# Kernel tuning notes

Hardware: AMD Instinct MI355X
Metric: run time of the kernel (lower is better)

## Reference

```python
import jax, jax.numpy as jnp
import numpy as np
import math

DIM = 1024
HEADS = 16
HEAD_DIM = DIM // HEADS
B, N = 1, 4096


def setup_inputs() -> dict:
    key = jax.random.key(0)
    k1, k2, k3, k4 = jax.random.split(key, 4)
    content = jax.random.normal(k1, (B, N, DIM), dtype=jnp.float32)
    # Original initializes projections as identity; perturb slightly so the
    # projections are non-trivial while staying well-conditioned.
    Wq = jnp.eye(DIM, dtype=jnp.float32) + 0.02 * jax.random.normal(k2, (DIM, DIM), dtype=jnp.float32)
    Wk = jnp.eye(DIM, dtype=jnp.float32) + 0.02 * jax.random.normal(k3, (DIM, DIM), dtype=jnp.float32)
    Wv = jnp.eye(DIM, dtype=jnp.float32) + 0.02 * jax.random.normal(k4, (DIM, DIM), dtype=jnp.float32)
    return {"content": content, "Wq": Wq, "Wk": Wk, "Wv": Wv}


def reference(content, Wq, Wk, Wv):
    b, n, d = content.shape
    # QKV projections: [B,N,D] @ [D,D]
    Q = (content @ Wq).reshape(b, n, HEADS, HEAD_DIM)
    K = (content @ Wk).reshape(b, n, HEADS, HEAD_DIM)
    V = (content @ Wv).reshape(b, n, HEADS, HEAD_DIM)
    # torch.split along the last dim == reshape into [.., HEADS, HEAD_DIM]
    scores = jnp.einsum('bqhd,bkhd->bhqk', Q, K) / math.sqrt(HEAD_DIM)
    alpha = jax.nn.softmax(scores, axis=-1)
    # Faithful to the original: masking zeroes the upper triangle AFTER the
    # softmax (no renormalization). With B=1 this applies to the whole batch,
    # exactly as the original loop (which only touches batch index 0).
    causal = jnp.tril(jnp.ones((n, n), dtype=bool))
    alpha = jnp.where(causal, alpha, jnp.zeros((), dtype=alpha.dtype))
    Y = jnp.einsum('bhqk,bkhd->bqhd', alpha, V).reshape(b, n, d)
    return Y
```

## Files before the change

### kernel.cpp

```cpp
#include <hip/hip_runtime.h>
#include <stdint.h>

#define DIMC 1024
#define NSEQ 4096
#define NH 16

typedef __attribute__((ext_vector_type(8))) short bf16x8;
typedef __attribute__((ext_vector_type(4))) float f32x4;

__device__ __forceinline__ unsigned short f2bf(float x) {
    union { float f; unsigned int u; } v; v.f = x;
    unsigned int u = v.u;
    return (unsigned short)((u + 0x7fffu + ((u >> 16) & 1u)) >> 16);
}

__global__ __launch_bounds__(256) void k_conv(const float* __restrict__ in,
                                              unsigned short* __restrict__ out) {
    int i = (blockIdx.x * 256 + threadIdx.x) * 8;
    float4 a = *reinterpret_cast<const float4*>(in + i);
    float4 b = *reinterpret_cast<const float4*>(in + i + 4);
    union { unsigned short us[8]; uint4 v; } r;
    r.us[0] = f2bf(a.x); r.us[1] = f2bf(a.y); r.us[2] = f2bf(a.z); r.us[3] = f2bf(a.w);
    r.us[4] = f2bf(b.x); r.us[5] = f2bf(b.y); r.us[6] = f2bf(b.z); r.us[7] = f2bf(b.w);
    *reinterpret_cast<uint4*>(out + i) = r.v;
}

__global__ __launch_bounds__(1024) void k_wt(const float* __restrict__ Wq,
                                             const float* __restrict__ Wk,
                                             const float* __restrict__ Wv,
                                             unsigned short* __restrict__ wt) {
    __shared__ float tile[32][33];
    int z = blockIdx.z;
    const float* W = (z == 0) ? Wq : ((z == 1) ? Wk : Wv);
    int n0 = blockIdx.x * 32, k0 = blockIdx.y * 32;
    tile[threadIdx.y][threadIdx.x] = W[(k0 + threadIdx.y) * DIMC + n0 + threadIdx.x];
    __syncthreads();
    wt[(size_t)z * DIMC * DIMC + (n0 + threadIdx.y) * DIMC + k0 + threadIdx.x] =
        f2bf(tile[threadIdx.x][threadIdx.y]);
}

__global__ __launch_bounds__(256) void k_gemm(const unsigned short* __restrict__ A,
                                              const unsigned short* __restrict__ Wt,
                                              unsigned short* __restrict__ Qb,
                                              unsigned short* __restrict__ Kb,
                                              unsigned short* __restrict__ Vt) {
    __shared__ unsigned short As[128][40];
    __shared__ unsigned short Bs[128][40];
    const int z = blockIdx.z;
    const unsigned short* Wz = Wt + (size_t)z * DIMC * DIMC;
    const int n0 = blockIdx.x * 128, m0 = blockIdx.y * 128;
    const int t = threadIdx.x;
    const int w = t >> 6, l = t & 63;
    const int wr = w >> 1, wc = w & 1;
    const int lq = l & 15, lg = l >> 4;
    const int srow = t >> 1, sch = (t & 1) * 16;

    f32x4 acc[4][4];
    #pragma unroll
    for (int i = 0; i < 4; ++i)
        #pragma unroll
        for (int j = 0; j < 4; ++j)
            acc[i][j] = f32x4{0.f, 0.f, 0.f, 0.f};

    for (int k0 = 0; k0 < DIMC; k0 += 32) {
        uint4 va0 = *reinterpret_cast<const uint4*>(A  + (m0 + srow) * DIMC + k0 + sch);
        uint4 va1 = *reinterpret_cast<const uint4*>(A  + (m0 + srow) * DIMC + k0 + sch + 8);
        uint4 vb0 = *reinterpret_cast<const uint4*>(Wz + (n0 + srow) * DIMC + k0 + sch);
        uint4 vb1 = *reinterpret_cast<const uint4*>(Wz + (n0 + srow) * DIMC + k0 + sch + 8);
        __syncthreads();
        *reinterpret_cast<uint4*>(&As[srow][sch])     = va0;
        *reinterpret_cast<uint4*>(&As[srow][sch + 8]) = va1;
        *reinterpret_cast<uint4*>(&Bs[srow][sch])     = vb0;
        *reinterpret_cast<uint4*>(&Bs[srow][sch + 8]) = vb1;
        __syncthreads();
        bf16x8 af[4], bfr[4];
        #pragma unroll
        for (int mf = 0; mf < 4; ++mf)
            af[mf] = *reinterpret_cast<const bf16x8*>(&As[wr * 64 + mf * 16 + lq][lg * 8]);
        #pragma unroll
        for (int nf = 0; nf < 4; ++nf)
            bfr[nf] = *reinterpret_cast<const bf16x8*>(&Bs[wc * 64 + nf * 16 + lq][lg * 8]);
        #pragma unroll
        for (int mf = 0; mf < 4; ++mf)
            #pragma unroll
            for (int nf = 0; nf < 4; ++nf)
                acc[mf][nf] = __builtin_amdgcn_mfma_f32_16x16x32_bf16(af[mf], bfr[nf], acc[mf][nf], 0, 0, 0);
    }

    if (z < 2) {
        unsigned short* out = (z == 0) ? Qb : Kb;
        #pragma unroll
        for (int mf = 0; mf < 4; ++mf)
            #pragma unroll
            for (int nf = 0; nf < 4; ++nf)
                #pragma unroll
                for (int j = 0; j < 4; ++j) {
                    int row = m0 + wr * 64 + mf * 16 + lg * 4 + j;
                    int col = n0 + wc * 64 + nf * 16 + lq;
                    out[row * DIMC + col] = f2bf(acc[mf][nf][j]);
                }
    } else {
        #pragma unroll
        for (int mf = 0; mf < 4; ++mf)
            #pragma unroll
            for (int nf = 0; nf < 4; ++nf) {
                int row  = n0 + wc * 64 + nf * 16 + lq;
                int colb = m0 + wr * 64 + mf * 16 + lg * 4;
                uint2 pk;
                pk.x = (unsigned)f2bf(acc[mf][nf][0]) | ((unsigned)f2bf(acc[mf][nf][1]) << 16);
                pk.y = (unsigned)f2bf(acc[mf][nf][2]) | ((unsigned)f2bf(acc[mf][nf][3]) << 16);
                *reinterpret_cast<uint2*>(Vt + (size_t)row * NSEQ + colb) = pk;
            }
    }
}

__global__ __launch_bounds__(256) void k_attn(const unsigned short* __restrict__ Qb,
                                              const unsigned short* __restrict__ Kb,
                                              const unsigned short* __restrict__ Vt,
                                              float* __restrict__ Y) {
    __shared__ unsigned short Ks[64][72];
    __shared__ unsigned short Vs[64][72];
    __shared__ unsigned short Ps[4][16][72];
    const int qb = blockIdx.x, h = blockIdx.y;
    const int t = threadIdx.x;
    const int w = t >> 6, l = t & 63;
    const int lq = l & 15, lg = l >> 4;

    bf16x8 qf0, qf1;
    {
        const unsigned short* qp = Qb + (qb * 64 + w * 16 + lq) * DIMC + h * 64 + lg * 8;
        qf0 = *reinterpret_cast<const bf16x8*>(qp);
        qf1 = *reinterpret_cast<const bf16x8*>(qp + 32);
    }
    float m_st = -__builtin_inff(), l_st = 0.f;
    float m_pv = -__builtin_inff();
    f32x4 O[4];
    #pragma unroll
    for (int df = 0; df < 4; ++df) O[df] = f32x4{0.f, 0.f, 0.f, 0.f};

    const int r0 = t >> 3, c0 = (t & 7) * 8;

    for (int kt = 0; kt < 64; ++kt) {
        const bool pv = (kt <= qb);
        uint4 kv0 = *reinterpret_cast<const uint4*>(Kb + (kt * 64 + r0) * DIMC + h * 64 + c0);
        uint4 kv1 = *reinterpret_cast<const uint4*>(Kb + (kt * 64 + 32 + r0) * DIMC + h * 64 + c0);
        uint4 vv0, vv1;
        if (pv) {
            vv0 = *reinterpret_cast<const uint4*>(Vt + (size_t)(h * 64 + r0) * NSEQ + kt * 64 + c0);
            vv1 = *reinterpret_cast<const uint4*>(Vt + (size_t)(h * 64 + 32 + r0) * NSEQ + kt * 64 + c0);
        }
        __syncthreads();
        *reinterpret_cast<uint4*>(&Ks[r0][c0])      = kv0;
        *reinterpret_cast<uint4*>(&Ks[32 + r0][c0]) = kv1;
        if (pv) {
            *reinterpret_cast<uint4*>(&Vs[r0][c0])      = vv0;
            *reinterpret_cast<uint4*>(&Vs[32 + r0][c0]) = vv1;
        }
        __syncthreads();

        f32x4 s[4];
        #pragma unroll
        for (int f = 0; f < 4; ++f) {
            s[f] = f32x4{0.f, 0.f, 0.f, 0.f};
            bf16x8 ka0 = *reinterpret_cast<const bf16x8*>(&Ks[f * 16 + lq][lg * 8]);
            bf16x8 ka1 = *reinterpret_cast<const bf16x8*>(&Ks[f * 16 + lq][32 + lg * 8]);
            s[f] = __builtin_amdgcn_mfma_f32_16x16x32_bf16(ka0, qf0, s[f], 0, 0, 0);
            s[f] = __builtin_amdgcn_mfma_f32_16x16x32_bf16(ka1, qf1, s[f], 0, 0, 0);
        }
        float tmax = -__builtin_inff();
        #pragma unroll
        for (int f = 0; f < 4; ++f)
            #pragma unroll
            for (int j = 0; j < 4; ++j) {
                s[f][j] *= 0.125f;
                tmax = fmaxf(tmax, s[f][j]);
            }
        tmax = fmaxf(tmax, __shfl_xor(tmax, 16));
        tmax = fmaxf(tmax, __shfl_xor(tmax, 32));
        const float mnew = fmaxf(m_st, tmax);
        const float sc = __expf(m_st - mnew);
        m_st = mnew;
        float p[4][4];
        float psum = 0.f;
        #pragma unroll
        for (int f = 0; f < 4; ++f)
            #pragma unroll
            for (int j = 0; j < 4; ++j) {
                p[f][j] = __expf(s[f][j] - mnew);
                psum += p[f][j];
            }
        psum += __shfl_xor(psum, 16);
        psum += __shfl_xor(psum, 32);
        l_st = l_st * sc + psum;

        if (pv) {
            m_pv = mnew;
            #pragma unroll
            for (int j = 0; j < 4; ++j) {
                const float scj = __shfl(sc, lg * 4 + j);
                #pragma unroll
                for (int df = 0; df < 4; ++df) O[df][j] *= scj;
            }
            const bool edge = (kt == qb);
            #pragma unroll
            for (int f = 0; f < 4; ++f) {
                float v0 = p[f][0], v1 = p[f][1], v2 = p[f][2], v3 = p[f][3];
                if (edge) {
                    const int kbase = f * 16 + lg * 4, qrel = w * 16 + lq;
                    if (kbase + 0 > qrel) v0 = 0.f;
                    if (kbase + 1 > qrel) v1 = 0.f;
                    if (kbase + 2 > qrel) v2 = 0.f;
                    if (kbase + 3 > qrel) v3 = 0.f;
                }
                uint2 pk;
                pk.x = (unsigned)f2bf(v0) | ((unsigned)f2bf(v1) << 16);
                pk.y = (unsigned)f2bf(v2) | ((unsigned)f2bf(v3) << 16);
                *reinterpret_cast<uint2*>(&Ps[w][lq][f * 16 + lg * 4]) = pk;
            }
            #pragma unroll
            for (int kk = 0; kk < 2; ++kk) {
                bf16x8 pa = *reinterpret_cast<const bf16x8*>(&Ps[w][lq][kk * 32 + lg * 8]);
                #pragma unroll
                for (int df = 0; df < 4; ++df) {
                    bf16x8 vb = *reinterpret_cast<const bf16x8*>(&Vs[df * 16 + lq][kk * 32 + lg * 8]);
                    O[df] = __builtin_amdgcn_mfma_f32_16x16x32_bf16(pa, vb, O[df], 0, 0, 0);
                }
            }
        }
    }

    const float corr = __expf(m_pv - m_st) / l_st;
    #pragma unroll
    for (int j = 0; j < 4; ++j) {
        const float li = __shfl(corr, lg * 4 + j);
        #pragma unroll
        for (int df = 0; df < 4; ++df)
            Y[(qb * 64 + w * 16 + lg * 4 + j) * DIMC + h * 64 + df * 16 + lq] = O[df][j] * li;
    }
}

extern "C" void kernel_launch(void* const* d_in, const int* in_sizes, int n_in,
                              void* d_out, int out_size, void* d_ws, size_t ws_size,
                              hipStream_t stream) {
    const float* content = (const float*)d_in[0];
    const float* Wq = (const float*)d_in[1];
    const float* Wk = (const float*)d_in[2];
    const float* Wv = (const float*)d_in[3];
    float* Y = (float*)d_out;
    unsigned short* ws  = (unsigned short*)d_ws;
    unsigned short* cbf = ws;
    unsigned short* wt  = cbf + (size_t)NSEQ * DIMC;
    unsigned short* qb  = wt  + (size_t)3 * DIMC * DIMC;
    unsigned short* kb  = qb  + (size_t)NSEQ * DIMC;
    unsigned short* vt  = kb  + (size_t)NSEQ * DIMC;

    hipLaunchKernelGGL(k_conv, dim3(NSEQ * DIMC / (256 * 8)), dim3(256), 0, stream, content, cbf);
    hipLaunchKernelGGL(k_wt,   dim3(32, 32, 3), dim3(32, 32), 0, stream, Wq, Wk, Wv, wt);
    hipLaunchKernelGGL(k_gemm, dim3(DIMC / 128, NSEQ / 128, 3), dim3(256), 0, stream, cbf, wt, qb, kb, vt);
    hipLaunchKernelGGL(k_attn, dim3(NSEQ / 64, NH), dim3(256), 0, stream, qb, kb, vt, Y);
}
```

Baseline: 285.6 us.

## Pair causal query tiles per block, prefetch K/V, lazy rescale, direct-to-LDS GEMM loads

```diff
diff --git a/kernel.cpp b/kernel.cpp
--- a/kernel.cpp
+++ b/kernel.cpp
@@ -4,6 +4,7 @@
 #define DIMC 1024
 #define NSEQ 4096
 #define NH 16
+#define QSCALE 0.18033688011112042f
 
 typedef __attribute__((ext_vector_type(8))) short bf16x8;
 typedef __attribute__((ext_vector_type(4))) float f32x4;
@@ -12,6 +13,18 @@
     union { float f; unsigned int u; } v; v.f = x;
     unsigned int u = v.u;
     return (unsigned short)((u + 0x7fffu + ((u >> 16) & 1u)) >> 16);
+}
+
+__device__ __forceinline__ unsigned cvt_pk_bf16(float lo, float hi) {
+    unsigned r;
+    asm("v_cvt_pk_bf16_f32 %0, %1, %2" : "=v"(r) : "v"(lo), "v"(hi));
+    return r;
+}
+
+__device__ __forceinline__ void gload16(const unsigned short* g, unsigned short* l) {
+    __builtin_amdgcn_global_load_lds(
+        (const __attribute__((address_space(1))) void*)g,
+        (__attribute__((address_space(3))) void*)l, 16, 0, 0);
 }
 
 __global__ __launch_bounds__(256) void k_conv(const float* __restrict__ in,
@@ -44,8 +57,8 @@
                                               unsigned short* __restrict__ Qb,
                                               unsigned short* __restrict__ Kb,
                                               unsigned short* __restrict__ Vt) {
-    __shared__ unsigned short As[128][40];
-    __shared__ unsigned short Bs[128][40];
+    __shared__ unsigned short As[128 * 32];
+    __shared__ unsigned short Bs[128 * 32];
     const int z = blockIdx.z;
     const unsigned short* Wz = Wt + (size_t)z * DIMC * DIMC;
     const int n0 = blockIdx.x * 128, m0 = blockIdx.y * 128;
@@ -53,7 +66,11 @@
     const int w = t >> 6, l = t & 63;
     const int wr = w >> 1, wc = w & 1;
     const int lq = l & 15, lg = l >> 4;
-    const int srow = t >> 1, sch = (t & 1) * 16;
+    const int srow = l >> 2, scol = (l & 3) * 8;
+    const unsigned short* gA = A  + (size_t)(m0 + w * 32 + srow) * DIMC + scol;
+    const unsigned short* gB = Wz + (size_t)(n0 + w * 32 + srow) * DIMC + scol;
+    unsigned short* lA = &As[(2 * w) * 512];
+    unsigned short* lB = &Bs[(2 * w) * 512];
 
     f32x4 acc[4][4];
     #pragma unroll
@@ -63,32 +80,31 @@
             acc[i][j] = f32x4{0.f, 0.f, 0.f, 0.f};
 
     for (int k0 = 0; k0 < DIMC; k0 += 32) {
-        uint4 va0 = *reinterpret_cast<const uint4*>(A  + (m0 + srow) * DIMC + k0 + sch);
-        uint4 va1 = *reinterpret_cast<const uint4*>(A  + (m0 + srow) * DIMC + k0 + sch + 8);
-        uint4 vb0 = *reinterpret_cast<const uint4*>(Wz + (n0 + srow) * DIMC + k0 + sch);
-        uint4 vb1 = *reinterpret_cast<const uint4*>(Wz + (n0 + srow) * DIMC + k0 + sch + 8);
-        __syncthreads();
-        *reinterpret_cast<uint4*>(&As[srow][sch])     = va0;
-        *reinterpret_cast<uint4*>(&As[srow][sch + 8]) = va1;
-        *reinterpret_cast<uint4*>(&Bs[srow][sch])     = vb0;
-        *reinterpret_cast<uint4*>(&Bs[srow][sch + 8]) = vb1;
+        __syncthreads();
+        gload16(gA + k0, lA);
+        gload16(gA + k0 + 16 * DIMC, lA + 512);
+        gload16(gB + k0, lB);
+        gload16(gB + k0 + 16 * DIMC, lB + 512);
         __syncthreads();
         bf16x8 af[4], bfr[4];
         #pragma unroll
         for (int mf = 0; mf < 4; ++mf)
-            af[mf] = *reinterpret_cast<const bf16x8*>(&As[wr * 64 + mf * 16 + lq][lg * 8]);
+            af[mf] = *reinterpret_cast<const bf16x8*>(&As[(wr * 64 + mf * 16 + lq) * 32 + lg * 8]);
         #pragma unroll
         for (int nf = 0; nf < 4; ++nf)
-            bfr[nf] = *reinterpret_cast<const bf16x8*>(&Bs[wc * 64 + nf * 16 + lq][lg * 8]);
+            bfr[nf] = *reinterpret_cast<const bf16x8*>(&Bs[(wc * 64 + nf * 16 + lq) * 32 + lg * 8]);
+        __builtin_amdgcn_s_setprio(1);
         #pragma unroll
         for (int mf = 0; mf < 4; ++mf)
             #pragma unroll
             for (int nf = 0; nf < 4; ++nf)
                 acc[mf][nf] = __builtin_amdgcn_mfma_f32_16x16x32_bf16(af[mf], bfr[nf], acc[mf][nf], 0, 0, 0);
+        __builtin_amdgcn_s_setprio(0);
     }
 
     if (z < 2) {
         unsigned short* out = (z == 0) ? Qb : Kb;
+        const float osc = (z == 0) ? QSCALE : 1.0f;
         #pragma unroll
         for (int mf = 0; mf < 4; ++mf)
             #pragma unroll
@@ -97,7 +113,7 @@
                 for (int j = 0; j < 4; ++j) {
                     int row = m0 + wr * 64 + mf * 16 + lg * 4 + j;
                     int col = n0 + wc * 64 + nf * 16 + lq;
-                    out[row * DIMC + col] = f2bf(acc[mf][nf][j]);
+                    out[row * DIMC + col] = f2bf(acc[mf][nf][j] * osc);
                 }
     } else {
         #pragma unroll
@@ -107,58 +123,58 @@
                 int row  = n0 + wc * 64 + nf * 16 + lq;
                 int colb = m0 + wr * 64 + mf * 16 + lg * 4;
                 uint2 pk;
-                pk.x = (unsigned)f2bf(acc[mf][nf][0]) | ((unsigned)f2bf(acc[mf][nf][1]) << 16);
-                pk.y = (unsigned)f2bf(acc[mf][nf][2]) | ((unsigned)f2bf(acc[mf][nf][3]) << 16);
+                pk.x = cvt_pk_bf16(acc[mf][nf][0], acc[mf][nf][1]);
+                pk.y = cvt_pk_bf16(acc[mf][nf][2], acc[mf][nf][3]);
                 *reinterpret_cast<uint2*>(Vt + (size_t)row * NSEQ + colb) = pk;
             }
     }
 }
 
-__global__ __launch_bounds__(256) void k_attn(const unsigned short* __restrict__ Qb,
-                                              const unsigned short* __restrict__ Kb,
-                                              const unsigned short* __restrict__ Vt,
-                                              float* __restrict__ Y) {
+__global__ __launch_bounds__(512, 4) void k_attn(const unsigned short* __restrict__ Qb,
+                                                 const unsigned short* __restrict__ Kb,
+                                                 const unsigned short* __restrict__ Vt,
+                                                 float* __restrict__ Y) {
     __shared__ unsigned short Ks[64][72];
     __shared__ unsigned short Vs[64][72];
-    __shared__ unsigned short Ps[4][16][72];
-    const int qb = blockIdx.x, h = blockIdx.y;
+    __shared__ unsigned short Ps[8][16][88];
+    const int bx = blockIdx.x, h = blockIdx.y;
     const int t = threadIdx.x;
     const int w = t >> 6, l = t & 63;
+    const int wq = w & 3, tile = w >> 2;
     const int lq = l & 15, lg = l >> 4;
+    const int qbA = bx, qbB = 63 - bx;
+    const int qb_my = tile ? qbB : qbA;
 
     bf16x8 qf0, qf1;
     {
-        const unsigned short* qp = Qb + (qb * 64 + w * 16 + lq) * DIMC + h * 64 + lg * 8;
+        const unsigned short* qp = Qb + (size_t)(qb_my * 64 + wq * 16 + lq) * DIMC + h * 64 + lg * 8;
         qf0 = *reinterpret_cast<const bf16x8*>(qp);
         qf1 = *reinterpret_cast<const bf16x8*>(qp + 32);
     }
-    float m_st = -__builtin_inff(), l_st = 0.f;
-    float m_pv = -__builtin_inff();
+    float m_fr = -__builtin_inff(), l_st = 0.f;
     f32x4 O[4];
     #pragma unroll
     for (int df = 0; df < 4; ++df) O[df] = f32x4{0.f, 0.f, 0.f, 0.f};
 
     const int r0 = t >> 3, c0 = (t & 7) * 8;
+    const unsigned short* gK = Kb + (size_t)r0 * DIMC + h * 64 + c0;
+    const unsigned short* gV = Vt + (size_t)(h * 64 + r0) * NSEQ + c0;
+
+    uint4 kv = *reinterpret_cast<const uint4*>(gK);
+    uint4 vv = *reinterpret_cast<const uint4*>(gV);
 
     for (int kt = 0; kt < 64; ++kt) {
-        const bool pv = (kt <= qb);
-        uint4 kv0 = *reinterpret_cast<const uint4*>(Kb + (kt * 64 + r0) * DIMC + h * 64 + c0);
-        uint4 kv1 = *reinterpret_cast<const uint4*>(Kb + (kt * 64 + 32 + r0) * DIMC + h * 64 + c0);
-        uint4 vv0, vv1;
-        if (pv) {
-            vv0 = *reinterpret_cast<const uint4*>(Vt + (size_t)(h * 64 + r0) * NSEQ + kt * 64 + c0);
-            vv1 = *reinterpret_cast<const uint4*>(Vt + (size_t)(h * 64 + 32 + r0) * NSEQ + kt * 64 + c0);
-        }
-        __syncthreads();
-        *reinterpret_cast<uint4*>(&Ks[r0][c0])      = kv0;
-        *reinterpret_cast<uint4*>(&Ks[32 + r0][c0]) = kv1;
-        if (pv) {
-            *reinterpret_cast<uint4*>(&Vs[r0][c0])      = vv0;
-            *reinterpret_cast<uint4*>(&Vs[32 + r0][c0]) = vv1;
-        }
-        __syncthreads();
+        __syncthreads();
+        *reinterpret_cast<uint4*>(&Ks[r0][c0]) = kv;
+        if (kt <= qbB) *reinterpret_cast<uint4*>(&Vs[r0][c0]) = vv;
+        __syncthreads();
+        if (kt < 63) {
+            kv = *reinterpret_cast<const uint4*>(gK + (size_t)(kt + 1) * 64 * DIMC);
+            if (kt + 1 <= qbB) vv = *reinterpret_cast<const uint4*>(gV + (kt + 1) * 64);
+        }
 
         f32x4 s[4];
+        __builtin_amdgcn_s_setprio(1);
         #pragma unroll
         for (int f = 0; f < 4; ++f) {
             s[f] = f32x4{0.f, 0.f, 0.f, 0.f};
@@ -167,56 +183,60 @@
             s[f] = __builtin_amdgcn_mfma_f32_16x16x32_bf16(ka0, qf0, s[f], 0, 0, 0);
             s[f] = __builtin_amdgcn_mfma_f32_16x16x32_bf16(ka1, qf1, s[f], 0, 0, 0);
         }
-        float tmax = -__builtin_inff();
+        __builtin_amdgcn_s_setprio(0);
+
+        float tmax = s[0][0];
         #pragma unroll
         for (int f = 0; f < 4; ++f)
             #pragma unroll
-            for (int j = 0; j < 4; ++j) {
-                s[f][j] *= 0.125f;
-                tmax = fmaxf(tmax, s[f][j]);
-            }
+            for (int j = 0; j < 4; ++j) tmax = fmaxf(tmax, s[f][j]);
         tmax = fmaxf(tmax, __shfl_xor(tmax, 16));
         tmax = fmaxf(tmax, __shfl_xor(tmax, 32));
-        const float mnew = fmaxf(m_st, tmax);
-        const float sc = __expf(m_st - mnew);
-        m_st = mnew;
-        float p[4][4];
+
+        if (!__all(tmax <= m_fr + 8.f)) {
+            const float mnew = fmaxf(m_fr, tmax);
+            const float sc = exp2f(m_fr - mnew);
+            l_st *= sc;
+            #pragma unroll
+            for (int j = 0; j < 4; ++j) {
+                const float scj = __shfl(sc, lg * 4 + j);
+                #pragma unroll
+                for (int df = 0; df < 4; ++df) O[df][j] *= scj;
+            }
+            m_fr = mnew;
+        }
         float psum = 0.f;
         #pragma unroll
         for (int f = 0; f < 4; ++f)
             #pragma unroll
             for (int j = 0; j < 4; ++j) {
-                p[f][j] = __expf(s[f][j] - mnew);
-                psum += p[f][j];
+                const float p = exp2f(s[f][j] - m_fr);
+                s[f][j] = p;
+                psum += p;
             }
         psum += __shfl_xor(psum, 16);
         psum += __shfl_xor(psum, 32);
-        l_st = l_st * sc + psum;
-
-        if (pv) {
-            m_pv = mnew;
-            #pragma unroll
-            for (int j = 0; j < 4; ++j) {
-                const float scj = __shfl(sc, lg * 4 + j);
-                #pragma unroll
-                for (int df = 0; df < 4; ++df) O[df][j] *= scj;
-            }
-            const bool edge = (kt == qb);
+        l_st += psum;
+
+        if (kt <= qb_my) {
+            if (kt == qb_my) {
+                const int qrel = wq * 16 + lq;
+                #pragma unroll
+                for (int f = 0; f < 4; ++f) {
+                    const int kbase = f * 16 + lg * 4;
+                    #pragma unroll
+                    for (int j = 0; j < 4; ++j)
+                        if (kbase + j > qrel) s[f][j] = 0.f;
+                }
+            }
             #pragma unroll
             for (int f = 0; f < 4; ++f) {
-                float v0 = p[f][0], v1 = p[f][1], v2 = p[f][2], v3 = p[f][3];
-                if (edge) {
-                    const int kbase = f * 16 + lg * 4, qrel = w * 16 + lq;
-                    if (kbase + 0 > qrel) v0 = 0.f;
-                    if (kbase + 1 > qrel) v1 = 0.f;
-                    if (kbase + 2 > qrel) v2 = 0.f;
-                    if (kbase + 3 > qrel) v3 = 0.f;
-                }
                 uint2 pk;
-                pk.x = (unsigned)f2bf(v0) | ((unsigned)f2bf(v1) << 16);
-                pk.y = (unsigned)f2bf(v2) | ((unsigned)f2bf(v3) << 16);
+                pk.x = cvt_pk_bf16(s[f][0], s[f][1]);
+                pk.y = cvt_pk_bf16(s[f][2], s[f][3]);
                 *reinterpret_cast<uint2*>(&Ps[w][lq][f * 16 + lg * 4]) = pk;
             }
+            __builtin_amdgcn_s_setprio(1);
             #pragma unroll
             for (int kk = 0; kk < 2; ++kk) {
                 bf16x8 pa = *reinterpret_cast<const bf16x8*>(&Ps[w][lq][kk * 32 + lg * 8]);
@@ -226,16 +246,17 @@
                     O[df] = __builtin_amdgcn_mfma_f32_16x16x32_bf16(pa, vb, O[df], 0, 0, 0);
                 }
             }
-        }
-    }
-
-    const float corr = __expf(m_pv - m_st) / l_st;
+            __builtin_amdgcn_s_setprio(0);
+        }
+    }
+
+    const float rl = 1.0f / l_st;
     #pragma unroll
     for (int j = 0; j < 4; ++j) {
-        const float li = __shfl(corr, lg * 4 + j);
+        const float li = __shfl(rl, lg * 4 + j);
         #pragma unroll
         for (int df = 0; df < 4; ++df)
-            Y[(qb * 64 + w * 16 + lg * 4 + j) * DIMC + h * 64 + df * 16 + lq] = O[df][j] * li;
+            Y[(qb_my * 64 + wq * 16 + lg * 4 + j) * DIMC + h * 64 + df * 16 + lq] = O[df][j] * li;
     }
 }
 
@@ -257,5 +278,5 @@
     hipLaunchKernelGGL(k_conv, dim3(NSEQ * DIMC / (256 * 8)), dim3(256), 0, stream, content, cbf);
     hipLaunchKernelGGL(k_wt,   dim3(32, 32, 3), dim3(32, 32), 0, stream, Wq, Wk, Wv, wt);
     hipLaunchKernelGGL(k_gemm, dim3(DIMC / 128, NSEQ / 128, 3), dim3(256), 0, stream, cbf, wt, qb, kb, vt);
-    hipLaunchKernelGGL(k_attn, dim3(NSEQ / 64, NH), dim3(256), 0, stream, qb, kb, vt, Y);
-}
+    hipLaunchKernelGGL(k_attn, dim3(NSEQ / 128, NH), dim3(512), 0, stream, qb, kb, vt, Y);
+}
```

New measurement: 258.7 us. 1.1x faster.
